# Performance work log

Measured on AMD Instinct MI355X. Metric: run time of the kernel, lower is better.

The kernel has to match this reference:

```python
import jax, jax.numpy as jnp
import numpy as np

N, E, IN, ED, H, C, G, NC = 50000, 800000, 128, 32, 4, 16, 64, 2
HC = H * C  # 64
NEG_SLOPE = 0.2
EPS = 1e-5


def _layernorm(x, g, b):
    mu = jnp.mean(x, axis=-1, keepdims=True)
    var = jnp.mean((x - mu) ** 2, axis=-1, keepdims=True)
    return (x - mu) * jax.lax.rsqrt(var + EPS) * g + b


def _gat(x, src, dst, edge_attr, W, a_src, a_dst, We, a_edge, b):
    """PyG GATConv (v1) with edge features, concat=True."""
    n = x.shape[0]
    h, c = a_src.shape
    xw = (x @ W).reshape(n, h, c)                       # [N,H,C]
    al_src = jnp.sum(xw * a_src, axis=-1)               # [N,H]
    al_dst = jnp.sum(xw * a_dst, axis=-1)               # [N,H]
    ew = (edge_attr @ We).reshape(-1, h, c)             # [Ef,H,C]
    al_e = jnp.sum(ew * a_edge, axis=-1)                # [Ef,H]
    alpha = al_src[src] + al_dst[dst] + al_e            # [Ef,H]
    alpha = jnp.where(alpha > 0, alpha, NEG_SLOPE * alpha)
    # segment softmax over incoming edges of each dst node
    amax = jax.ops.segment_max(alpha, dst, num_segments=n)
    amax = jnp.where(jnp.isfinite(amax), amax, 0.0)
    ex = jnp.exp(alpha - amax[dst])
    denom = jax.ops.segment_sum(ex, dst, num_segments=n)
    att = ex / (denom[dst] + 1e-16)                     # [Ef,H]
    msg = xw[src] * att[:, :, None]                     # [Ef,H,C]
    out = jax.ops.segment_sum(msg, dst, num_segments=n) # [N,H,C]
    return out.reshape(n, h * c) + b


def setup_inputs() -> dict:
    ks = jax.random.split(jax.random.key(0), 24)
    s = 0.1
    inp = {
        "x": jax.random.normal(ks[0], (N, IN), jnp.float32),
        "edge_attr": jax.random.normal(ks[1], (E, ED), jnp.float32),
        "W1": jax.random.normal(ks[2], (IN, HC), jnp.float32) * s,
        "as1": jax.random.normal(ks[3], (H, C), jnp.float32) * s,
        "ad1": jax.random.normal(ks[4], (H, C), jnp.float32) * s,
        "We1": jax.random.normal(ks[5], (ED, HC), jnp.float32) * s,
        "ae1": jax.random.normal(ks[6], (H, C), jnp.float32) * s,
        "b1": jnp.zeros((HC,), jnp.float32),
        "W2": jax.random.normal(ks[7], (HC, HC), jnp.float32) * s,
        "as2": jax.random.normal(ks[8], (H, C), jnp.float32) * s,
        "ad2": jax.random.normal(ks[9], (H, C), jnp.float32) * s,
        "We2": jax.random.normal(ks[10], (ED, HC), jnp.float32) * s,
        "ae2": jax.random.normal(ks[11], (H, C), jnp.float32) * s,
        "b2": jnp.zeros((HC,), jnp.float32),
        "g1": jnp.ones((HC,), jnp.float32),
        "be1": jnp.zeros((HC,), jnp.float32),
        "fw1": jax.random.normal(ks[12], (HC, 32), jnp.float32) * s,
        "fb1": jnp.zeros((32,), jnp.float32),
        "g2": jnp.ones((32,), jnp.float32),
        "be2": jnp.zeros((32,), jnp.float32),
        "fw2": jax.random.normal(ks[13], (32, NC), jnp.float32) * s,
        "fb2": jnp.zeros((NC,), jnp.float32),
        "edge_index": jax.random.randint(ks[14], (2, E), 0, N, jnp.int64),
        "batch": jnp.sort(jax.random.randint(ks[15], (N,), 0, G, jnp.int64)),
    }
    return inp


def reference(x, edge_attr, W1, as1, ad1, We1, ae1, b1, W2, as2, ad2, We2, ae2,
              b2, g1, be1, fw1, fb1, g2, be2, fw2, fb2, edge_index, batch):
    src, dst = edge_index[0], edge_index[1]
    e = edge_attr.shape[0]
    # add_self_loops with fill_value='mean' (mean of incoming edge_attr per node)
    cnt = jax.ops.segment_sum(jnp.ones((e,), x.dtype), dst, num_segments=N)
    loop_ea = jax.ops.segment_sum(edge_attr, dst, num_segments=N) / jnp.clip(cnt, 1.0)[:, None]
    ar = jnp.arange(N)
    src_f = jnp.concatenate([src, ar])
    dst_f = jnp.concatenate([dst, ar])
    ea_f = jnp.concatenate([edge_attr, loop_ea], axis=0)

    h = _gat(x, src_f, dst_f, ea_f, W1, as1, ad1, We1, ae1, b1)
    h = jax.nn.relu(h)
    h = _layernorm(h, g1, be1)
    h = _gat(h, src_f, dst_f, ea_f, W2, as2, ad2, We2, ae2, b2)
    h = jax.nn.relu(h)
    pooled = jax.ops.segment_max(h, batch, num_segments=G)   # global_max_pool
    pooled = jnp.where(jnp.isfinite(pooled), pooled, 0.0)
    z = pooled @ fw1 + fb1
    z = _layernorm(z, g2, be2)
    z = jax.nn.relu(z)
    # dropout(p=0.4) is identity in eval mode
    z = z @ fw2 + fb2
    return jax.nn.log_softmax(z, axis=1)
```

## Files before the change

kernel.cpp:

```cpp
#include <hip/hip_runtime.h>
#include <math.h>

#define N_NODES 50000
#define N_EDGES 800000
#define IN_DIM 128
#define ED_DIM 32
#define NH 4
#define CH 16
#define HC 64
#define NG 64
#define NCL 2
#define NEG_SLOPE 0.2f
#define LN_EPS 1e-5f
#define NBLK1 196

__global__ void k_hist(const int* __restrict__ dst, int* __restrict__ cnt,
                       int* __restrict__ rank_e) {
    int e = blockIdx.x * 256 + threadIdx.x;
    if (e < N_EDGES) rank_e[e] = atomicAdd(&cnt[dst[e]], 1);
}

__global__ void k_scan_local(const int* __restrict__ cnt, int* __restrict__ tmp_ex,
                             int* __restrict__ bsum) {
    __shared__ int sd[256];
    int t = threadIdx.x, idx = blockIdx.x * 256 + t;
    int v = (idx < N_NODES) ? cnt[idx] : 0;
    sd[t] = v; __syncthreads();
    for (int off = 1; off < 256; off <<= 1) {
        int add = (t >= off) ? sd[t - off] : 0;
        __syncthreads();
        sd[t] += add;
        __syncthreads();
    }
    if (idx < N_NODES) tmp_ex[idx] = sd[t] - v;
    if (t == 255) bsum[blockIdx.x] = sd[t];
}

__global__ void k_scan_final(const int* __restrict__ tmp_ex, const int* __restrict__ bsum,
                             int* __restrict__ row_start) {
    __shared__ int sd[256];
    int t = threadIdx.x;
    int v = (t < NBLK1) ? bsum[t] : 0;
    sd[t] = v; __syncthreads();
    for (int off = 1; off < 256; off <<= 1) {
        int add = (t >= off) ? sd[t - off] : 0;
        __syncthreads();
        sd[t] += add;
        __syncthreads();
    }
    int boff = sd[blockIdx.x] - bsum[blockIdx.x];
    int idx = blockIdx.x * 256 + t;
    if (idx < N_NODES) row_start[idx] = tmp_ex[idx] + boff;
    if (idx == 0) row_start[N_NODES] = N_EDGES;
}

__global__ void k_edge_lin(const float* __restrict__ ea,
                           const float* __restrict__ We1, const float* __restrict__ ae1,
                           const float* __restrict__ We2, const float* __restrict__ ae2,
                           float4* __restrict__ ale8) {
    __shared__ float sVe[ED_DIM * 8];
    int t = threadIdx.x;
    {
        int d = t >> 3, k = t & 7;
        int l = k >> 2, h = k & 3;
        const float* We = l ? We2 : We1;
        const float* ae = l ? ae2 : ae1;
        float s = 0.f;
        #pragma unroll
        for (int c = 0; c < CH; ++c) s += We[d * HC + h * CH + c] * ae[h * CH + c];
        sVe[d * 8 + k] = s;
    }
    __syncthreads();
    int e = blockIdx.x * 256 + t;
    if (e >= N_EDGES) return;
    float a[8];
    #pragma unroll
    for (int k = 0; k < 8; ++k) a[k] = 0.f;
    const float4* er4 = (const float4*)(ea + (long long)e * ED_DIM);
    #pragma unroll
    for (int q = 0; q < ED_DIM / 4; ++q) {
        float4 v = er4[q];
        float ev[4] = {v.x, v.y, v.z, v.w};
        #pragma unroll
        for (int u = 0; u < 4; ++u) {
            #pragma unroll
            for (int k = 0; k < 8; ++k) a[k] += ev[u] * sVe[(q * 4 + u) * 8 + k];
        }
    }
    float4* out = ale8 + (long long)e * 2;
    out[0] = make_float4(a[0], a[1], a[2], a[3]);
    out[1] = make_float4(a[4], a[5], a[6], a[7]);
}

__global__ void k_perm2(const int* __restrict__ dst, const int* __restrict__ srcI,
                        const int* __restrict__ rank_e, const int* __restrict__ row_start,
                        int2* __restrict__ perm_src) {
    int e = blockIdx.x * 256 + threadIdx.x;
    if (e >= N_EDGES) return;
    int pos = row_start[dst[e]] + rank_e[e];
    perm_src[pos] = make_int2(e, srcI[e]);
}

template<int K>
__global__ void k_xw(const float* __restrict__ X, const float* __restrict__ W,
                     const float* __restrict__ AS, const float* __restrict__ AD,
                     float* __restrict__ XW, float* __restrict__ ALS, float* __restrict__ ALD) {
    __shared__ float sW[K * HC];
    __shared__ float sX[16 * K];
    int t = threadIdx.x;
    for (int i = t; i < K * HC; i += 256) sW[i] = W[i];
    int nb = blockIdx.x * 16;
    for (int i = t; i < 16 * K; i += 256) sX[i] = X[(long long)nb * K + i];
    __syncthreads();
    int sub = t >> 6, j = t & 63;
    float acc[4] = {0.f, 0.f, 0.f, 0.f};
    #pragma unroll 8
    for (int k = 0; k < K; ++k) {
        float wv = sW[k * HC + j];
        #pragma unroll
        for (int q = 0; q < 4; ++q) acc[q] += sX[(sub + 4 * q) * K + k] * wv;
    }
    float as_ = AS[j], ad_ = AD[j];
    #pragma unroll
    for (int q = 0; q < 4; ++q) {
        int n = nb + sub + 4 * q;
        XW[(long long)n * HC + j] = acc[q];
        float vs = acc[q] * as_, vd = acc[q] * ad_;
        #pragma unroll
        for (int m = 1; m < 16; m <<= 1) { vs += __shfl_xor(vs, m); vd += __shfl_xor(vd, m); }
        if ((j & 15) == 0) {
            int h = j >> 4;
            ALS[n * 4 + h] = vs; ALD[n * 4 + h] = vd;
        }
    }
}

template<bool DO_LN, int LOFF>
__global__ void k_agg(const int* __restrict__ rs, const int2* __restrict__ ps,
                      const float* __restrict__ ale8,
                      const float* __restrict__ ALS, const float* __restrict__ ALD,
                      const float* __restrict__ XW, const float* __restrict__ bias,
                      const float* __restrict__ gam, const float* __restrict__ bet,
                      float* __restrict__ OUT) {
    int n = (blockIdx.x * blockDim.x + threadIdx.x) >> 6;
    if (n >= N_NODES) return;
    int lane = threadIdx.x & 63;
    int h = lane >> 4;
    int e0 = rs[n], e1 = rs[n + 1];
    float adn = ALD[n * 4 + h];
    float acc0 = 0.f, l0 = 0.f, as0 = 0.f;
    float acc1 = 0.f, l1 = 0.f, as1 = 0.f;
    float acc2 = 0.f, l2 = 0.f, as2 = 0.f;
    float acc3 = 0.f, l3 = 0.f, as3 = 0.f;
    int e = e0;
    for (; e + 3 < e1; e += 4) {
        int2 pA = ps[e], pB = ps[e + 1], pC = ps[e + 2], pD = ps[e + 3];
        float aeA = ale8[(long long)pA.x * 8 + LOFF + h];
        float aeB = ale8[(long long)pB.x * 8 + LOFF + h];
        float aeC = ale8[(long long)pC.x * 8 + LOFF + h];
        float aeD = ale8[(long long)pD.x * 8 + LOFF + h];
        float xA = XW[pA.y * HC + lane];
        float xB = XW[pB.y * HC + lane];
        float xC = XW[pC.y * HC + lane];
        float xD = XW[pD.y * HC + lane];
        float aA = ALS[pA.y * 4 + h] + adn + aeA;
        float aB = ALS[pB.y * 4 + h] + adn + aeB;
        float aC = ALS[pC.y * 4 + h] + adn + aeC;
        float aD = ALS[pD.y * 4 + h] + adn + aeD;
        aA = aA > 0.f ? aA : NEG_SLOPE * aA;
        aB = aB > 0.f ? aB : NEG_SLOPE * aB;
        aC = aC > 0.f ? aC : NEG_SLOPE * aC;
        aD = aD > 0.f ? aD : NEG_SLOPE * aD;
        float qA = __expf(aA), qB = __expf(aB), qC = __expf(aC), qD = __expf(aD);
        acc0 += qA * xA; l0 += qA; as0 += aeA;
        acc1 += qB * xB; l1 += qB; as1 += aeB;
        acc2 += qC * xC; l2 += qC; as2 += aeC;
        acc3 += qD * xD; l3 += qD; as3 += aeD;
    }
    for (; e < e1; ++e) {
        int2 pA = ps[e];
        float aeA = ale8[(long long)pA.x * 8 + LOFF + h];
        float xA = XW[pA.y * HC + lane];
        float aA = ALS[pA.y * 4 + h] + adn + aeA;
        aA = aA > 0.f ? aA : NEG_SLOPE * aA;
        float qA = __expf(aA);
        acc0 += qA * xA; l0 += qA; as0 += aeA;
    }
    int d = e1 - e0;
    float invd = 1.f / (float)(d > 0 ? d : 1);
    float aSelf = ALS[n * 4 + h] + adn + (as0 + as1 + as2 + as3) * invd;
    aSelf = aSelf > 0.f ? aSelf : NEG_SLOPE * aSelf;
    float pS = __expf(aSelf);
    float acc = (acc0 + acc1) + (acc2 + acc3) + pS * XW[n * HC + lane];
    float l = (l0 + l1) + (l2 + l3) + pS;
    float v = acc / (l + 1e-16f) + bias[lane];
    v = fmaxf(v, 0.f);
    if (DO_LN) {
        float s1 = v;
        #pragma unroll
        for (int mm = 1; mm < 64; mm <<= 1) s1 += __shfl_xor(s1, mm);
        float mean = s1 * (1.f / 64.f);
        float dd = v - mean;
        float s2 = dd * dd;
        #pragma unroll
        for (int mm = 1; mm < 64; mm <<= 1) s2 += __shfl_xor(s2, mm);
        float var = s2 * (1.f / 64.f);
        v = dd * rsqrtf(var + LN_EPS) * gam[lane] + bet[lane];
    }
    OUT[(long long)n * HC + lane] = v;
}

__global__ void k_pool(const float* __restrict__ H2, const int* __restrict__ batch,
                       float* __restrict__ pooled) {
    int j = threadIdx.x & 63;
    int r = threadIdx.x >> 6;
    int base = blockIdx.x * 128;
    int gcur = -1; float rm = 0.f;
    for (int n = base + r; n < base + 128 && n < N_NODES; n += 4) {
        int g = batch[n];
        if (g != gcur) {
            if (gcur >= 0) atomicMax((unsigned int*)&pooled[gcur * HC + j], __float_as_uint(rm));
            gcur = g; rm = 0.f;
        }
        rm = fmaxf(rm, H2[(long long)n * HC + j]);
    }
    if (gcur >= 0) atomicMax((unsigned int*)&pooled[gcur * HC + j], __float_as_uint(rm));
}

__global__ void k_head(const float* __restrict__ pooled,
                       const float* __restrict__ fw1, const float* __restrict__ fb1,
                       const float* __restrict__ g2, const float* __restrict__ be2,
                       const float* __restrict__ fw2, const float* __restrict__ fb2,
                       float* __restrict__ out) {
    int g = blockIdx.x;
    int j = threadIdx.x;
    float z = 0.f;
    if (j < 32) {
        for (int k = 0; k < HC; ++k) z += pooled[g * HC + k] * fw1[k * 32 + j];
        z += fb1[j];
    }
    float s1 = (j < 32) ? z : 0.f;
    for (int m = 1; m < 32; m <<= 1) s1 += __shfl_xor(s1, m, 32);
    float mean = s1 * (1.f / 32.f);
    float d = z - mean;
    float s2 = (j < 32) ? d * d : 0.f;
    for (int m = 1; m < 32; m <<= 1) s2 += __shfl_xor(s2, m, 32);
    float var = s2 * (1.f / 32.f);
    float zz = 0.f;
    if (j < 32) {
        zz = d * rsqrtf(var + LN_EPS) * g2[j] + be2[j];
        zz = fmaxf(zz, 0.f);
    }
    float p0 = (j < 32) ? zz * fw2[j * NCL + 0] : 0.f;
    float p1 = (j < 32) ? zz * fw2[j * NCL + 1] : 0.f;
    for (int m = 1; m < 32; m <<= 1) { p0 += __shfl_xor(p0, m, 32); p1 += __shfl_xor(p1, m, 32); }
    if (j == 0) {
        float l0 = p0 + fb2[0], l1 = p1 + fb2[1];
        float mx = fmaxf(l0, l1);
        float ls = mx + logf(__expf(l0 - mx) + __expf(l1 - mx));
        out[g * NCL + 0] = l0 - ls;
        out[g * NCL + 1] = l1 - ls;
    }
}

extern "C" void kernel_launch(void* const* d_in, const int* in_sizes, int n_in,
                              void* d_out, int out_size, void* d_ws, size_t ws_size,
                              hipStream_t stream) {
    const float* x   = (const float*)d_in[0];
    const float* ea  = (const float*)d_in[1];
    const float* W1  = (const float*)d_in[2];
    const float* as1 = (const float*)d_in[3];
    const float* ad1 = (const float*)d_in[4];
    const float* We1 = (const float*)d_in[5];
    const float* ae1 = (const float*)d_in[6];
    const float* b1  = (const float*)d_in[7];
    const float* W2  = (const float*)d_in[8];
    const float* as2 = (const float*)d_in[9];
    const float* ad2 = (const float*)d_in[10];
    const float* We2 = (const float*)d_in[11];
    const float* ae2 = (const float*)d_in[12];
    const float* b2  = (const float*)d_in[13];
    const float* g1  = (const float*)d_in[14];
    const float* be1 = (const float*)d_in[15];
    const float* fw1 = (const float*)d_in[16];
    const float* fb1 = (const float*)d_in[17];
    const float* g2  = (const float*)d_in[18];
    const float* be2 = (const float*)d_in[19];
    const float* fw2 = (const float*)d_in[20];
    const float* fb2 = (const float*)d_in[21];
    const int* eidx  = (const int*)d_in[22];
    const int* batch = (const int*)d_in[23];
    const int* srcI = eidx;
    const int* dstI = eidx + N_EDGES;

    char* w = (char*)d_ws;
    auto alloc = [&](size_t bytes) { char* p = w; w += (bytes + 255) & ~(size_t)255; return p; };
    int*   cnt       = (int*)  alloc((size_t)N_NODES * 4);
    int*   row_start = (int*)  alloc((size_t)(N_NODES + 1) * 4);
    int*   rank_e    = (int*)  alloc((size_t)N_EDGES * 4);
    int*   tmp_ex    = (int*)  alloc((size_t)N_NODES * 4);
    int*   bsum      = (int*)  alloc(256 * 4);
    int2*  perm_src  = (int2*) alloc((size_t)N_EDGES * 8);
    float4* ale8     = (float4*)alloc((size_t)N_EDGES * 32);
    float* xw1       = (float*)alloc((size_t)N_NODES * HC * 4);
    float* als1      = (float*)alloc((size_t)N_NODES * 4 * 4);
    float* ald1      = (float*)alloc((size_t)N_NODES * 4 * 4);
    float* h1        = (float*)alloc((size_t)N_NODES * HC * 4);
    float* als2      = (float*)alloc((size_t)N_NODES * 4 * 4);
    float* ald2      = (float*)alloc((size_t)N_NODES * 4 * 4);
    float* pooled    = (float*)alloc((size_t)NG * HC * 4);
    float* xw2 = xw1;
    float* h2  = h1;

    hipMemsetAsync(cnt, 0, (size_t)N_NODES * 4, stream);
    hipMemsetAsync(pooled, 0, (size_t)NG * HC * 4, stream);

    k_hist<<<N_EDGES / 256, 256, 0, stream>>>(dstI, cnt, rank_e);
    k_scan_local<<<NBLK1, 256, 0, stream>>>(cnt, tmp_ex, bsum);
    k_scan_final<<<NBLK1, 256, 0, stream>>>(tmp_ex, bsum, row_start);
    k_edge_lin<<<N_EDGES / 256, 256, 0, stream>>>(ea, We1, ae1, We2, ae2, ale8);
    k_perm2<<<N_EDGES / 256, 256, 0, stream>>>(dstI, srcI, rank_e, row_start, perm_src);

    k_xw<IN_DIM><<<N_NODES / 16, 256, 0, stream>>>(x, W1, as1, ad1, xw1, als1, ald1);
    k_agg<true, 0><<<N_NODES / 4, 256, 0, stream>>>(row_start, perm_src, (const float*)ale8,
                                                    als1, ald1, xw1, b1, g1, be1, h1);
    k_xw<HC><<<N_NODES / 16, 256, 0, stream>>>(h1, W2, as2, ad2, xw2, als2, ald2);
    k_agg<false, 4><<<N_NODES / 4, 256, 0, stream>>>(row_start, perm_src, (const float*)ale8,
                                                     als2, ald2, xw2, b2, nullptr, nullptr, h2);

    k_pool<<<(N_NODES + 127) / 128, 256, 0, stream>>>(h2, batch, pooled);
    k_head<<<NG, 64, 0, stream>>>(pooled, fw1, fb1, g2, be2, fw2, fb2, (float*)d_out);
}
```

Measured before the change: 458.4 us.

## Fuse histogram, edge projection and first node matmul into one multi-job kernel

Merges the edge histogram, the edge-attribute attention projection and the layer-1 node linear transform into one kernel, with blocks interleaved by job id. It also merges the final scan with the CSR permutation scatter by recomputing block offsets in shared memory. The aim is to cut launch count and let independent memory-bound and compute work overlap on the GPU. In exchange every block now reserves the large shared-memory footprint of the matmul job, which may lower occupancy for the lighter edge jobs.

```diff
diff --git a/kernel.cpp b/kernel.cpp
--- a/kernel.cpp
+++ b/kernel.cpp
@@ -13,12 +13,8 @@
 #define NEG_SLOPE 0.2f
 #define LN_EPS 1e-5f
 #define NBLK1 196
-
-__global__ void k_hist(const int* __restrict__ dst, int* __restrict__ cnt,
-                       int* __restrict__ rank_e) {
-    int e = blockIdx.x * 256 + threadIdx.x;
-    if (e < N_EDGES) rank_e[e] = atomicAdd(&cnt[dst[e]], 1);
-}
+#define NB_TILE 3125
+#define NB_ECH 3125
 
 __global__ void k_scan_local(const int* __restrict__ cnt, int* __restrict__ tmp_ex,
                              int* __restrict__ bsum) {
@@ -36,9 +32,92 @@
     if (t == 255) bsum[blockIdx.x] = sd[t];
 }
 
-__global__ void k_scan_final(const int* __restrict__ tmp_ex, const int* __restrict__ bsum,
-                             int* __restrict__ row_start) {
+__global__ __launch_bounds__(256) void k_phase1(
+        const float* __restrict__ X, const float* __restrict__ W,
+        const float* __restrict__ AS, const float* __restrict__ AD,
+        float* __restrict__ XW, float* __restrict__ ALS, float* __restrict__ ALD,
+        const float* __restrict__ ea,
+        const float* __restrict__ We1, const float* __restrict__ ae1,
+        const float* __restrict__ We2, const float* __restrict__ ae2,
+        float4* __restrict__ ale8,
+        const int* __restrict__ dst, int* __restrict__ cnt, int* __restrict__ rank_e) {
+    __shared__ float smem[IN_DIM * HC + 16 * IN_DIM];
+    int job = blockIdx.x % 3;
+    int bid = blockIdx.x / 3;
+    int t = threadIdx.x;
+    if (job == 0) {
+        const int K = IN_DIM;
+        float* sW = smem;
+        float* sX = smem + K * HC;
+        for (int i = t; i < K * HC; i += 256) sW[i] = W[i];
+        int nb = bid * 16;
+        for (int i = t; i < 16 * K; i += 256) sX[i] = X[(long long)nb * K + i];
+        __syncthreads();
+        int sub = t >> 6, j = t & 63;
+        float acc[4] = {0.f, 0.f, 0.f, 0.f};
+        #pragma unroll 8
+        for (int k = 0; k < K; ++k) {
+            float wv = sW[k * HC + j];
+            #pragma unroll
+            for (int q = 0; q < 4; ++q) acc[q] += sX[(sub + 4 * q) * K + k] * wv;
+        }
+        float as_ = AS[j], ad_ = AD[j];
+        #pragma unroll
+        for (int q = 0; q < 4; ++q) {
+            int n = nb + sub + 4 * q;
+            XW[(long long)n * HC + j] = acc[q];
+            float vs = acc[q] * as_, vd = acc[q] * ad_;
+            #pragma unroll
+            for (int m = 1; m < 16; m <<= 1) { vs += __shfl_xor(vs, m); vd += __shfl_xor(vd, m); }
+            if ((j & 15) == 0) {
+                int h = j >> 4;
+                ALS[n * 4 + h] = vs; ALD[n * 4 + h] = vd;
+            }
+        }
+    } else if (job == 1) {
+        float* sVe = smem;
+        {
+            int d = t >> 3, k = t & 7;
+            int l = k >> 2, h = k & 3;
+            const float* We = l ? We2 : We1;
+            const float* ae = l ? ae2 : ae1;
+            float s = 0.f;
+            #pragma unroll
+            for (int c = 0; c < CH; ++c) s += We[d * HC + h * CH + c] * ae[h * CH + c];
+            sVe[d * 8 + k] = s;
+        }
+        __syncthreads();
+        int e = bid * 256 + t;
+        if (e >= N_EDGES) return;
+        float a[8];
+        #pragma unroll
+        for (int k = 0; k < 8; ++k) a[k] = 0.f;
+        const float4* er4 = (const float4*)(ea + (long long)e * ED_DIM);
+        #pragma unroll
+        for (int q = 0; q < ED_DIM / 4; ++q) {
+            float4 v = er4[q];
+            float ev[4] = {v.x, v.y, v.z, v.w};
+            #pragma unroll
+            for (int u = 0; u < 4; ++u) {
+                #pragma unroll
+                for (int k = 0; k < 8; ++k) a[k] += ev[u] * sVe[(q * 4 + u) * 8 + k];
+            }
+        }
+        float4* out = ale8 + (long long)e * 2;
+        out[0] = make_float4(a[0], a[1], a[2], a[3]);
+        out[1] = make_float4(a[4], a[5], a[6], a[7]);
+    } else {
+        int e = bid * 256 + t;
+        if (e < N_EDGES) rank_e[e] = atomicAdd(&cnt[dst[e]], 1);
+    }
+}
+
+__global__ void k_scan_perm(const int* __restrict__ tmp_ex, const int* __restrict__ bsum,
+                            int* __restrict__ row_start,
+                            const int* __restrict__ dst, const int* __restrict__ srcI,
+                            const int* __restrict__ rank_e, int2* __restrict__ perm_src) {
     __shared__ int sd[256];
+    __shared__ int sboff[256];
     int t = threadIdx.x;
     int v = (t < NBLK1) ? bsum[t] : 0;
     sd[t] = v; __syncthreads();
@@ -48,57 +127,20 @@
         sd[t] += add;
         __syncthreads();
     }
-    int boff = sd[blockIdx.x] - bsum[blockIdx.x];
-    int idx = blockIdx.x * 256 + t;
-    if (idx < N_NODES) row_start[idx] = tmp_ex[idx] + boff;
-    if (idx == 0) row_start[N_NODES] = N_EDGES;
-}
-
-__global__ void k_edge_lin(const float* __restrict__ ea,
-                           const float* __restrict__ We1, const float* __restrict__ ae1,
-                           const float* __restrict__ We2, const float* __restrict__ ae2,
-                           float4* __restrict__ ale8) {
-    __shared__ float sVe[ED_DIM * 8];
-    int t = threadIdx.x;
-    {
-        int d = t >> 3, k = t & 7;
-        int l = k >> 2, h = k & 3;
-        const float* We = l ? We2 : We1;
-        const float* ae = l ? ae2 : ae1;
-        float s = 0.f;
-        #pragma unroll
-        for (int c = 0; c < CH; ++c) s += We[d * HC + h * CH + c] * ae[h * CH + c];
-        sVe[d * 8 + k] = s;
-    }
+    sboff[t] = sd[t] - v;
     __syncthreads();
-    int e = blockIdx.x * 256 + t;
-    if (e >= N_EDGES) return;
-    float a[8];
-    #pragma unroll
-    for (int k = 0; k < 8; ++k) a[k] = 0.f;
-    const float4* er4 = (const float4*)(ea + (long long)e * ED_DIM);
-    #pragma unroll
-    for (int q = 0; q < ED_DIM / 4; ++q) {
-        float4 v = er4[q];
-        float ev[4] = {v.x, v.y, v.z, v.w};
-        #pragma unroll
-        for (int u = 0; u < 4; ++u) {
-            #pragma unroll
-            for (int k = 0; k < 8; ++k) a[k] += ev[u] * sVe[(q * 4 + u) * 8 + k];
-        }
-    }
-    float4* out = ale8 + (long long)e * 2;
-    out[0] = make_float4(a[0], a[1], a[2], a[3]);
-    out[1] = make_float4(a[4], a[5], a[6], a[7]);
-}
-
-__global__ void k_perm2(const int* __restrict__ dst, const int* __restrict__ srcI,
-                        const int* __restrict__ rank_e, const int* __restrict__ row_start,
-                        int2* __restrict__ perm_src) {
-    int e = blockIdx.x * 256 + threadIdx.x;
-    if (e >= N_EDGES) return;
-    int pos = row_start[dst[e]] + rank_e[e];
-    perm_src[pos] = make_int2(e, srcI[e]);
+    if (blockIdx.x < NBLK1) {
+        int idx = blockIdx.x * 256 + t;
+        if (idx < N_NODES) row_start[idx] = tmp_ex[idx] + sboff[blockIdx.x];
+        if (idx == 0) row_start[N_NODES] = N_EDGES;
+    } else {
+        int e = (blockIdx.x - NBLK1) * 256 + t;
+        if (e < N_EDGES) {
+            int d = dst[e];
+            int pos = tmp_ex[d] + sboff[d >> 8] + rank_e[e];
+            perm_src[pos] = make_int2(e, srcI[e]);
+        }
+    }
 }
 
 template<int K>
@@ -315,13 +357,13 @@
     hipMemsetAsync(cnt, 0, (size_t)N_NODES * 4, stream);
     hipMemsetAsync(pooled, 0, (size_t)NG * HC * 4, stream);
 
-    k_hist<<<N_EDGES / 256, 256, 0, stream>>>(dstI, cnt, rank_e);
+    k_phase1<<<3 * NB_TILE, 256, 0, stream>>>(x, W1, as1, ad1, xw1, als1, ald1,
+                                              ea, We1, ae1, We2, ae2, ale8,
+                                              dstI, cnt, rank_e);
     k_scan_local<<<NBLK1, 256, 0, stream>>>(cnt, tmp_ex, bsum);
-    k_scan_final<<<NBLK1, 256, 0, stream>>>(tmp_ex, bsum, row_start);
-    k_edge_lin<<<N_EDGES / 256, 256, 0, stream>>>(ea, We1, ae1, We2, ae2, ale8);
-    k_perm2<<<N_EDGES / 256, 256, 0, stream>>>(dstI, srcI, rank_e, row_start, perm_src);
-
-    k_xw<IN_DIM><<<N_NODES / 16, 256, 0, stream>>>(x, W1, as1, ad1, xw1, als1, ald1);
+    k_scan_perm<<<NBLK1 + NB_ECH, 256, 0, stream>>>(tmp_ex, bsum, row_start,
+                                                    dstI, srcI, rank_e, perm_src);
+
     k_agg<true, 0><<<N_NODES / 4, 256, 0, stream>>>(row_start, perm_src, (const float*)ale8,
                                                     als1, ald1, xw1, b1, g1, be1, h1);
     k_xw<HC><<<N_NODES / 16, 256, 0, stream>>>(h1, W2, as2, ad2, xw2, als2, ald2);
```

Result: faster. 418.6 us (-8.7%).
